# Optimization experiments

Hardware: AMD Instinct MI355X
Metric: run time of the kernel (lower is better)

Reference implementation:

```python
import jax, jax.numpy as jnp
import numpy as np

S, B, M, F, C = 32, 128, 128, 512, 100


def setup_inputs() -> dict:
    key = jax.random.key(0)
    k = jax.random.split(key, 7)
    x = jax.random.normal(k[0], (B, F), dtype=jnp.float32)
    y = jax.random.randint(k[1], (B,), 0, C, dtype=jnp.int32)
    # Z in {-1, +1}: Bernoulli(0.5) sample mapped via 2*b - 1 (mirrors sample_Z)
    Zb = (jax.random.uniform(k[2], (S, B, M)) < 0.5).astype(jnp.float32)
    Z = 2.0 * Zb - 1.0
    alpha_0 = jax.random.normal(k[3], (M,), dtype=jnp.float32)
    init_c = 2.0 / np.sqrt(F)
    alpha = init_c * jax.random.normal(k[4], (M, F), dtype=jnp.float32)
    alpha = alpha / jnp.linalg.norm(alpha, axis=0, keepdims=True)
    beta_0 = jax.random.normal(k[5], (C,), dtype=jnp.float32)
    init_c2 = 2.0 / np.sqrt(M)
    beta = init_c2 * jax.random.normal(k[6], (C, M), dtype=jnp.float32)
    return {"x": x, "y": y, "Z": Z, "alpha_0": alpha_0, "alpha": alpha,
            "beta_0": beta_0, "beta": beta}


def reference(x, y, Z, alpha_0, alpha, beta_0, beta):
    # linear_eta / eta (compute_linear_eta, compute_eta)
    linear_eta = alpha_0[None, :] + x @ alpha.T            # [B, M]
    eta = jax.nn.sigmoid(linear_eta)                        # exp(l)/(1+exp(l))

    y_onehot = jax.nn.one_hot(y, C, dtype=Z.dtype)          # [B, C]
    # Unperturbed logits shared across all j (rank-1 structure of compute_pi_j)
    base = beta_0[None, None, :] + jnp.einsum('sbm,cm->sbc', Z, beta)  # [S,B,C]

    def pi_for(target):
        # Flipping column j of Z to `target` shifts logits by (target - Z_j)*beta[:, j]
        delta = (target - Z)[..., None] * beta.T[None, None, :, :]  # [S,B,M,C]
        lin = base[:, :, None, :] + delta                            # [S,B,M,C]
        # NOTE: original ADDS the max (faithful to source); softmax ratio unchanged
        lin = lin + jnp.max(lin, axis=-1, keepdims=True)
        num = jnp.sum(y_onehot[None, :, None, :] * lin, axis=-1)     # [S,B,M]
        den = jnp.sum(jnp.exp(lin), axis=-1)                         # [S,B,M]
        return jnp.exp(num) / den                                    # [S,B,M]

    pi_pos = pi_for(1.0)
    pi_neg = pi_for(-1.0)
    # compute_EY_X_j: sum over Monte-Carlo samples
    EY_X_j = jnp.sum(pi_pos * eta[None] + pi_neg * (1.0 - eta)[None], axis=0)  # [B,M]
    return EY_X_j
```

## Files before the change

### kernel.cpp

```cpp
#include <hip/hip_runtime.h>
#include <math.h>

#define S_ 32
#define B_ 128
#define M_ 128
#define F_ 512
#define C_ 100
#define RWZ 136
#define RWE 120

typedef _Float16 f16;
typedef _Float16 f16x2 __attribute__((ext_vector_type(2)));
typedef _Float16 f16x4 __attribute__((ext_vector_type(4)));
typedef _Float16 f16x8 __attribute__((ext_vector_type(8)));
typedef float f32x4 __attribute__((ext_vector_type(4)));

__global__ __launch_bounds__(512) void k_main(
    const float* __restrict__ x, const int* __restrict__ y,
    const float* __restrict__ Z, const float* __restrict__ alpha0,
    const float* __restrict__ alpha, const float* __restrict__ beta0,
    const float* __restrict__ beta, float* __restrict__ out) {
  const int b = blockIdx.x;
  const int tid = threadIdx.x;
  const int lane = tid & 63;
  const int w = tid >> 6;
  const int l15 = lane & 15;
  const int lg = lane >> 4;

  __shared__ f16 Zf[S_ * RWZ];
  __shared__ f16 BT[112 * RWZ];
  __shared__ f16 EPT[M_ * RWE];
  __shared__ f16 ENT[M_ * RWE];
  __shared__ float baseS[S_ * 112];
  __shared__ f16 Pt[S_ * RWE];
  __shared__ float etaS[M_];
  __shared__ float PybS[S_];

  const int yb = y[b];

  {
    const float4* Z4 = (const float4*)Z;
#pragma unroll
    for (int i4 = tid; i4 < 1024; i4 += 512) {
      int p = i4 >> 5;
      int mj = (i4 & 31) * 4;
      float4 v = Z4[((size_t)p * B_ + b) * 32 + (i4 & 31)];
      f16x4 h = {(f16)v.x, (f16)v.y, (f16)v.z, (f16)v.w};
      *(f16x4*)&Zf[p * RWZ + mj] = h;
    }
    const float4* be4 = (const float4*)beta;
    for (int i4 = tid; i4 < 3200; i4 += 512) {
      int c = i4 >> 5;
      int mj = (i4 & 31) * 4;
      float4 v = be4[i4];
      f16x4 h = {(f16)v.x, (f16)v.y, (f16)v.z, (f16)v.w};
      *(f16x4*)&BT[c * RWZ + mj] = h;
    }
    for (int i = tid; i < 12 * RWZ; i += 512) BT[100 * RWZ + i] = (f16)0.f;
  }
  __syncthreads();

  {
    for (int i = tid; i < 8192; i += 512) {
      int c = i & 127;
      int m2 = (i >> 7) << 1;
      if (c < 112) {
        float ep0 = 0.f, en0 = 0.f, ep1 = 0.f, en1 = 0.f;
        if (c < C_) {
          f16x2 bb = *(const f16x2*)&BT[c * RWZ + m2];
          float b0 = (float)bb[0], b1 = (float)bb[1];
          ep0 = __expf(2.f * b0); en0 = __expf(-2.f * b0);
          ep1 = __expf(2.f * b1); en1 = __expf(-2.f * b1);
        }
        EPT[m2 * RWE + c] = (f16)ep0; EPT[(m2 + 1) * RWE + c] = (f16)ep1;
        ENT[m2 * RWE + c] = (f16)en0; ENT[(m2 + 1) * RWE + c] = (f16)en1;
      }
    }
    const float4* x4 = (const float4*)x;
    const float4* a4 = (const float4*)alpha;
    float4 xr[8];
#pragma unroll
    for (int r = 0; r < 8; ++r) xr[r] = x4[b * 128 + r * 16 + l15];
#pragma unroll
    for (int j = 0; j < 4; ++j) {
      int m = w * 16 + j * 4 + lg;
      float acc = 0.f;
#pragma unroll
      for (int r = 0; r < 8; ++r) {
        float4 av = a4[(size_t)m * 128 + r * 16 + l15];
        float4 xv = xr[r];
        acc = fmaf(av.x, xv.x, acc); acc = fmaf(av.y, xv.y, acc);
        acc = fmaf(av.z, xv.z, acc); acc = fmaf(av.w, xv.w, acc);
      }
      acc += __shfl_xor(acc, 1);
      acc += __shfl_xor(acc, 2);
      acc += __shfl_xor(acc, 4);
      acc += __shfl_xor(acc, 8);
      if (l15 == 0) {
        float l = alpha0[m] + acc;
        etaS[m] = 1.f / (1.f + __expf(-l));
      }
    }
  }
  __syncthreads();

  if (w < 7) {
    f32x4 acc0 = {0.f, 0.f, 0.f, 0.f}, acc1 = {0.f, 0.f, 0.f, 0.f};
    const char* ZfB = (const char*)Zf;
    const char* BTB = (const char*)BT;
#pragma unroll
    for (int kc = 0; kc < 4; ++kc) {
      int ko = kc * 64 + lg * 16;
      f16x8 a0 = *(const f16x8*)(ZfB + l15 * (RWZ * 2) + ko);
      f16x8 a1 = *(const f16x8*)(ZfB + (16 + l15) * (RWZ * 2) + ko);
      f16x8 bb = *(const f16x8*)(BTB + (w * 16 + l15) * (RWZ * 2) + ko);
      acc0 = __builtin_amdgcn_mfma_f32_16x16x32_f16(a0, bb, acc0, 0, 0, 0);
      acc1 = __builtin_amdgcn_mfma_f32_16x16x32_f16(a1, bb, acc1, 0, 0, 0);
    }
    int col = w * 16 + l15;
    float b0v = (col < C_) ? beta0[col] : 0.f;
#pragma unroll
    for (int j = 0; j < 4; ++j) {
      baseS[(lg * 4 + j) * 112 + col] = acc0[j] + b0v;
      baseS[(16 + lg * 4 + j) * 112 + col] = acc1[j] + b0v;
    }
  }
  __syncthreads();

  {
#pragma unroll
    for (int k = 0; k < 4; ++k) {
      int p = w * 4 + k;
      float v1 = baseS[p * 112 + lane];
      float v2 = (lane < 36) ? baseS[p * 112 + 64 + lane] : -1e30f;
      float mx = fmaxf(v1, v2);
#pragma unroll
      for (int off = 32; off > 0; off >>= 1) mx = fmaxf(mx, __shfl_xor(mx, off));
      float e1 = __expf(v1 - mx);
      float e2 = (lane < 36) ? __expf(v2 - mx) : 0.f;
      float sm = e1 + e2;
#pragma unroll
      for (int off = 32; off > 0; off >>= 1) sm += __shfl_xor(sm, off);
      float rd = 1.f / sm;
      Pt[p * RWE + lane] = (f16)(e1 * rd);
      if (lane < 48) Pt[p * RWE + 64 + lane] = (f16)(lane < 36 ? e2 * rd : 0.f);
      if (lane == yb) PybS[p] = e1 * rd;
      if (lane + 64 == yb) PybS[p] = e2 * rd;
    }
  }
  __syncthreads();

  {
    f32x4 pAcc0 = {0.f,0.f,0.f,0.f}, pAcc1 = {0.f,0.f,0.f,0.f};
    f32x4 nAcc0 = {0.f,0.f,0.f,0.f}, nAcc1 = {0.f,0.f,0.f,0.f};
    const char* PtB = (const char*)Pt;
    const char* EPB = (const char*)EPT;
    const char* ENB = (const char*)ENT;
#pragma unroll
    for (int kc = 0; kc < 3; ++kc) {
      int ko = kc * 64 + lg * 16;
      f16x8 a0 = *(const f16x8*)(PtB + l15 * (RWE * 2) + ko);
      f16x8 a1 = *(const f16x8*)(PtB + (16 + l15) * (RWE * 2) + ko);
      f16x8 bp = *(const f16x8*)(EPB + (w * 16 + l15) * (RWE * 2) + ko);
      f16x8 bn = *(const f16x8*)(ENB + (w * 16 + l15) * (RWE * 2) + ko);
      pAcc0 = __builtin_amdgcn_mfma_f32_16x16x32_f16(a0, bp, pAcc0, 0, 0, 0);
      pAcc1 = __builtin_amdgcn_mfma_f32_16x16x32_f16(a1, bp, pAcc1, 0, 0, 0);
      nAcc0 = __builtin_amdgcn_mfma_f32_16x16x32_f16(a0, bn, nAcc0, 0, 0, 0);
      nAcc1 = __builtin_amdgcn_mfma_f32_16x16x32_f16(a1, bn, nAcc1, 0, 0, 0);
    }
    {
      int ko3 = 192 + lg * 8;
      f16x4 a0 = *(const f16x4*)(PtB + l15 * (RWE * 2) + ko3);
      f16x4 a1 = *(const f16x4*)(PtB + (16 + l15) * (RWE * 2) + ko3);
      f16x4 bp = *(const f16x4*)(EPB + (w * 16 + l15) * (RWE * 2) + ko3);
      f16x4 bn = *(const f16x4*)(ENB + (w * 16 + l15) * (RWE * 2) + ko3);
      pAcc0 = __builtin_amdgcn_mfma_f32_16x16x16f16(a0, bp, pAcc0, 0, 0, 0);
      pAcc1 = __builtin_amdgcn_mfma_f32_16x16x16f16(a1, bp, pAcc1, 0, 0, 0);
      nAcc0 = __builtin_amdgcn_mfma_f32_16x16x16f16(a0, bn, nAcc0, 0, 0, 0);
      nAcc1 = __builtin_amdgcn_mfma_f32_16x16x16f16(a1, bn, nAcc1, 0, 0, 0);
    }
    int m = w * 16 + l15;
    float epy = (float)EPT[m * RWE + yb];
    float eny = (float)ENT[m * RWE + yb];
    float eta_v = etaS[m];
    float ome = 1.f - eta_v;
    float o = 0.f;
#pragma unroll
    for (int j = 0; j < 4; ++j) {
      {
        int p = lg * 4 + j;
        float z = (float)Zf[p * RWZ + m];
        float pyb = PybS[p];
        o += (z > 0.f) ? fmaf(pyb, eta_v, (pyb * eny / nAcc0[j]) * ome)
                       : fmaf(pyb * epy / pAcc0[j], eta_v, pyb * ome);
      }
      {
        int p = 16 + lg * 4 + j;
        float z = (float)Zf[p * RWZ + m];
        float pyb = PybS[p];
        o += (z > 0.f) ? fmaf(pyb, eta_v, (pyb * eny / nAcc1[j]) * ome)
                       : fmaf(pyb * epy / pAcc1[j], eta_v, pyb * ome);
      }
    }
    o += __shfl_xor(o, 16);
    o += __shfl_xor(o, 32);
    if (lane < 16) out[b * M_ + w * 16 + lane] = o;
  }
}

extern "C" void kernel_launch(void* const* d_in, const int* in_sizes, int n_in,
                              void* d_out, int out_size, void* d_ws, size_t ws_size,
                              hipStream_t stream) {
  const float* x = (const float*)d_in[0];
  const int* y = (const int*)d_in[1];
  const float* Z = (const float*)d_in[2];
  const float* alpha0 = (const float*)d_in[3];
  const float* alpha = (const float*)d_in[4];
  const float* beta0 = (const float*)d_in[5];
  const float* beta = (const float*)d_in[6];
  float* out = (float*)d_out;

  k_main<<<dim3(B_), dim3(512), 0, stream>>>(x, y, Z, alpha0, alpha, beta0,
                                             beta, out);
}
```

Baseline: 17.77 us.

## Split into precompute kernel and S-split main kernel with atomic accumulation

Moves the beta-to-f16 conversion, the exp(±2β) tables and the eta computation out of the per-batch block into a separate pre-kernel that writes them to workspace, so they are computed once instead of once per block. The main kernel is then split across two blocks per batch row, each handling 16 samples, and the two halves are combined with atomicAdd into an output zeroed by a memset. This doubles the grid and shrinks shared memory per block, which should help occupancy. The cost is two extra launches (memset and pre-kernel), a workspace round-trip, reading the B tables from global memory instead of LDS, and atomics on the output.

```diff
diff --git a/kernel.cpp b/kernel.cpp
--- a/kernel.cpp
+++ b/kernel.cpp
@@ -15,72 +15,25 @@
 typedef _Float16 f16x8 __attribute__((ext_vector_type(8)));
 typedef float f32x4 __attribute__((ext_vector_type(4)));
 
-__global__ __launch_bounds__(512) void k_main(
-    const float* __restrict__ x, const int* __restrict__ y,
-    const float* __restrict__ Z, const float* __restrict__ alpha0,
-    const float* __restrict__ alpha, const float* __restrict__ beta0,
-    const float* __restrict__ beta, float* __restrict__ out) {
-  const int b = blockIdx.x;
+#define WS_BT   0
+#define WS_EPT  30720
+#define WS_ENT  61440
+#define WS_ETA  92160
+
+__global__ __launch_bounds__(512) void k_pre(
+    const float* __restrict__ x, const float* __restrict__ alpha0,
+    const float* __restrict__ alpha, const float* __restrict__ beta,
+    char* __restrict__ ws) {
+  const int bid = blockIdx.x;
   const int tid = threadIdx.x;
-  const int lane = tid & 63;
-  const int w = tid >> 6;
-  const int l15 = lane & 15;
-  const int lg = lane >> 4;
-
-  __shared__ f16 Zf[S_ * RWZ];
-  __shared__ f16 BT[112 * RWZ];
-  __shared__ f16 EPT[M_ * RWE];
-  __shared__ f16 ENT[M_ * RWE];
-  __shared__ float baseS[S_ * 112];
-  __shared__ f16 Pt[S_ * RWE];
-  __shared__ float etaS[M_];
-  __shared__ float PybS[S_];
-
-  const int yb = y[b];
-
-  {
-    const float4* Z4 = (const float4*)Z;
-#pragma unroll
-    for (int i4 = tid; i4 < 1024; i4 += 512) {
-      int p = i4 >> 5;
-      int mj = (i4 & 31) * 4;
-      float4 v = Z4[((size_t)p * B_ + b) * 32 + (i4 & 31)];
-      f16x4 h = {(f16)v.x, (f16)v.y, (f16)v.z, (f16)v.w};
-      *(f16x4*)&Zf[p * RWZ + mj] = h;
-    }
-    const float4* be4 = (const float4*)beta;
-    for (int i4 = tid; i4 < 3200; i4 += 512) {
-      int c = i4 >> 5;
-      int mj = (i4 & 31) * 4;
-      float4 v = be4[i4];
-      f16x4 h = {(f16)v.x, (f16)v.y, (f16)v.z, (f16)v.w};
-      *(f16x4*)&BT[c * RWZ + mj] = h;
-    }
-    for (int i = tid; i < 12 * RWZ; i += 512) BT[100 * RWZ + i] = (f16)0.f;
-  }
-  __syncthreads();
-
-  {
-    for (int i = tid; i < 8192; i += 512) {
-      int c = i & 127;
-      int m2 = (i >> 7) << 1;
-      if (c < 112) {
-        float ep0 = 0.f, en0 = 0.f, ep1 = 0.f, en1 = 0.f;
-        if (c < C_) {
-          f16x2 bb = *(const f16x2*)&BT[c * RWZ + m2];
-          float b0 = (float)bb[0], b1 = (float)bb[1];
-          ep0 = __expf(2.f * b0); en0 = __expf(-2.f * b0);
-          ep1 = __expf(2.f * b1); en1 = __expf(-2.f * b1);
-        }
-        EPT[m2 * RWE + c] = (f16)ep0; EPT[(m2 + 1) * RWE + c] = (f16)ep1;
-        ENT[m2 * RWE + c] = (f16)en0; ENT[(m2 + 1) * RWE + c] = (f16)en1;
-      }
-    }
+  if (bid < B_) {
+    float* etag = (float*)(ws + WS_ETA);
+    const int lane = tid & 63, w = tid >> 6, l15 = lane & 15, lg = lane >> 4;
     const float4* x4 = (const float4*)x;
     const float4* a4 = (const float4*)alpha;
     float4 xr[8];
 #pragma unroll
-    for (int r = 0; r < 8; ++r) xr[r] = x4[b * 128 + r * 16 + l15];
+    for (int r = 0; r < 8; ++r) xr[r] = x4[bid * 128 + r * 16 + l15];
 #pragma unroll
     for (int j = 0; j < 4; ++j) {
       int m = w * 16 + j * 4 + lg;
@@ -98,39 +51,85 @@
       acc += __shfl_xor(acc, 8);
       if (l15 == 0) {
         float l = alpha0[m] + acc;
-        etaS[m] = 1.f / (1.f + __expf(-l));
+        etag[bid * 128 + m] = 1.f / (1.f + __expf(-l));
       }
     }
+  } else {
+    f16* BTg = (f16*)(ws + WS_BT);
+    f16* EPTg = (f16*)(ws + WS_EPT);
+    f16* ENTg = (f16*)(ws + WS_ENT);
+    const int base = (bid - B_) * 512;
+    for (int i = base + tid; i < C_ * M_; i += 4 * 512) {
+      int c = i >> 7, m = i & 127;
+      float bv = beta[i];
+      BTg[c * RWZ + m] = (f16)bv;
+      EPTg[m * RWE + c] = (f16)__expf(2.f * bv);
+      ENTg[m * RWE + c] = (f16)__expf(-2.f * bv);
+    }
+    for (int i = base + tid; i < 12 * RWZ; i += 4 * 512) BTg[100 * RWZ + i] = (f16)0.f;
+    for (int i = base + tid; i < 128 * 32; i += 4 * 512) {
+      int m = i >> 5, k = i & 31;
+      if (k < 20) { EPTg[m * RWE + 100 + k] = (f16)0.f; ENTg[m * RWE + 100 + k] = (f16)0.f; }
+    }
+  }
+}
+
+__global__ __launch_bounds__(512) void k_main(
+    const float* __restrict__ Z, const int* __restrict__ y,
+    const float* __restrict__ beta0, const char* __restrict__ ws,
+    float* __restrict__ out) {
+  const int sh = blockIdx.x;
+  const int b = blockIdx.y;
+  const int tid = threadIdx.x;
+  const int lane = tid & 63;
+  const int w = tid >> 6;
+  const int l15 = lane & 15;
+  const int lg = lane >> 4;
+
+  const f16* BTg = (const f16*)(ws + WS_BT);
+  const f16* EPTg = (const f16*)(ws + WS_EPT);
+  const f16* ENTg = (const f16*)(ws + WS_ENT);
+  const float* etag = (const float*)(ws + WS_ETA);
+
+  __shared__ f16 Zf[16 * RWZ];
+  __shared__ float baseS[16 * 112];
+  __shared__ f16 Pt[16 * RWE];
+  __shared__ float PybS[16];
+
+  const int yb = y[b];
+
+  {
+    int p = tid >> 5, q = tid & 31;
+    float4 v = ((const float4*)Z)[((size_t)(sh * 16 + p) * B_ + b) * 32 + q];
+    f16x4 h = {(f16)v.x, (f16)v.y, (f16)v.z, (f16)v.w};
+    *(f16x4*)&Zf[p * RWZ + q * 4] = h;
   }
   __syncthreads();
 
   if (w < 7) {
-    f32x4 acc0 = {0.f, 0.f, 0.f, 0.f}, acc1 = {0.f, 0.f, 0.f, 0.f};
+    const char* BTB = (const char*)BTg;
     const char* ZfB = (const char*)Zf;
-    const char* BTB = (const char*)BT;
+    f16x8 bfr[4];
+#pragma unroll
+    for (int kc = 0; kc < 4; ++kc)
+      bfr[kc] = *(const f16x8*)(BTB + (w * 16 + l15) * (RWZ * 2) + kc * 64 + lg * 16);
+    f32x4 acc = {0.f, 0.f, 0.f, 0.f};
 #pragma unroll
     for (int kc = 0; kc < 4; ++kc) {
-      int ko = kc * 64 + lg * 16;
-      f16x8 a0 = *(const f16x8*)(ZfB + l15 * (RWZ * 2) + ko);
-      f16x8 a1 = *(const f16x8*)(ZfB + (16 + l15) * (RWZ * 2) + ko);
-      f16x8 bb = *(const f16x8*)(BTB + (w * 16 + l15) * (RWZ * 2) + ko);
-      acc0 = __builtin_amdgcn_mfma_f32_16x16x32_f16(a0, bb, acc0, 0, 0, 0);
-      acc1 = __builtin_amdgcn_mfma_f32_16x16x32_f16(a1, bb, acc1, 0, 0, 0);
+      f16x8 a0 = *(const f16x8*)(ZfB + l15 * (RWZ * 2) + kc * 64 + lg * 16);
+      acc = __builtin_amdgcn_mfma_f32_16x16x32_f16(a0, bfr[kc], acc, 0, 0, 0);
     }
     int col = w * 16 + l15;
     float b0v = (col < C_) ? beta0[col] : 0.f;
 #pragma unroll
-    for (int j = 0; j < 4; ++j) {
-      baseS[(lg * 4 + j) * 112 + col] = acc0[j] + b0v;
-      baseS[(16 + lg * 4 + j) * 112 + col] = acc1[j] + b0v;
-    }
+    for (int j = 0; j < 4; ++j) baseS[(lg * 4 + j) * 112 + col] = acc[j] + b0v;
   }
   __syncthreads();
 
   {
 #pragma unroll
-    for (int k = 0; k < 4; ++k) {
-      int p = w * 4 + k;
+    for (int k = 0; k < 2; ++k) {
+      int p = w * 2 + k;
       float v1 = baseS[p * 112 + lane];
       float v2 = (lane < 36) ? baseS[p * 112 + 64 + lane] : -1e30f;
       float mx = fmaxf(v1, v2);
@@ -151,60 +150,47 @@
   __syncthreads();
 
   {
-    f32x4 pAcc0 = {0.f,0.f,0.f,0.f}, pAcc1 = {0.f,0.f,0.f,0.f};
-    f32x4 nAcc0 = {0.f,0.f,0.f,0.f}, nAcc1 = {0.f,0.f,0.f,0.f};
     const char* PtB = (const char*)Pt;
-    const char* EPB = (const char*)EPT;
-    const char* ENB = (const char*)ENT;
+    const char* EPB = (const char*)EPTg;
+    const char* ENB = (const char*)ENTg;
+    const int rowoff = (w * 16 + l15) * (RWE * 2);
+    f16x8 bp[3], bn[3];
 #pragma unroll
     for (int kc = 0; kc < 3; ++kc) {
-      int ko = kc * 64 + lg * 16;
-      f16x8 a0 = *(const f16x8*)(PtB + l15 * (RWE * 2) + ko);
-      f16x8 a1 = *(const f16x8*)(PtB + (16 + l15) * (RWE * 2) + ko);
-      f16x8 bp = *(const f16x8*)(EPB + (w * 16 + l15) * (RWE * 2) + ko);
-      f16x8 bn = *(const f16x8*)(ENB + (w * 16 + l15) * (RWE * 2) + ko);
-      pAcc0 = __builtin_amdgcn_mfma_f32_16x16x32_f16(a0, bp, pAcc0, 0, 0, 0);
-      pAcc1 = __builtin_amdgcn_mfma_f32_16x16x32_f16(a1, bp, pAcc1, 0, 0, 0);
-      nAcc0 = __builtin_amdgcn_mfma_f32_16x16x32_f16(a0, bn, nAcc0, 0, 0, 0);
-      nAcc1 = __builtin_amdgcn_mfma_f32_16x16x32_f16(a1, bn, nAcc1, 0, 0, 0);
+      bp[kc] = *(const f16x8*)(EPB + rowoff + kc * 64 + lg * 16);
+      bn[kc] = *(const f16x8*)(ENB + rowoff + kc * 64 + lg * 16);
+    }
+    f16x4 bp3 = *(const f16x4*)(EPB + rowoff + 192 + lg * 8);
+    f16x4 bn3 = *(const f16x4*)(ENB + rowoff + 192 + lg * 8);
+    f32x4 pA = {0.f, 0.f, 0.f, 0.f}, nA = {0.f, 0.f, 0.f, 0.f};
+#pragma unroll
+    for (int kc = 0; kc < 3; ++kc) {
+      f16x8 a0 = *(const f16x8*)(PtB + l15 * (RWE * 2) + kc * 64 + lg * 16);
+      pA = __builtin_amdgcn_mfma_f32_16x16x32_f16(a0, bp[kc], pA, 0, 0, 0);
+      nA = __builtin_amdgcn_mfma_f32_16x16x32_f16(a0, bn[kc], nA, 0, 0, 0);
     }
     {
-      int ko3 = 192 + lg * 8;
-      f16x4 a0 = *(const f16x4*)(PtB + l15 * (RWE * 2) + ko3);
-      f16x4 a1 = *(const f16x4*)(PtB + (16 + l15) * (RWE * 2) + ko3);
-      f16x4 bp = *(const f16x4*)(EPB + (w * 16 + l15) * (RWE * 2) + ko3);
-      f16x4 bn = *(const f16x4*)(ENB + (w * 16 + l15) * (RWE * 2) + ko3);
-      pAcc0 = __builtin_amdgcn_mfma_f32_16x16x16f16(a0, bp, pAcc0, 0, 0, 0);
-      pAcc1 = __builtin_amdgcn_mfma_f32_16x16x16f16(a1, bp, pAcc1, 0, 0, 0);
-      nAcc0 = __builtin_amdgcn_mfma_f32_16x16x16f16(a0, bn, nAcc0, 0, 0, 0);
-      nAcc1 = __builtin_amdgcn_mfma_f32_16x16x16f16(a1, bn, nAcc1, 0, 0, 0);
+      f16x4 a3 = *(const f16x4*)(PtB + l15 * (RWE * 2) + 192 + lg * 8);
+      pA = __builtin_amdgcn_mfma_f32_16x16x16f16(a3, bp3, pA, 0, 0, 0);
+      nA = __builtin_amdgcn_mfma_f32_16x16x16f16(a3, bn3, nA, 0, 0, 0);
     }
     int m = w * 16 + l15;
-    float epy = (float)EPT[m * RWE + yb];
-    float eny = (float)ENT[m * RWE + yb];
-    float eta_v = etaS[m];
+    float epy = (float)EPTg[m * RWE + yb];
+    float eny = (float)ENTg[m * RWE + yb];
+    float eta_v = etag[b * M_ + m];
     float ome = 1.f - eta_v;
     float o = 0.f;
 #pragma unroll
     for (int j = 0; j < 4; ++j) {
-      {
-        int p = lg * 4 + j;
-        float z = (float)Zf[p * RWZ + m];
-        float pyb = PybS[p];
-        o += (z > 0.f) ? fmaf(pyb, eta_v, (pyb * eny / nAcc0[j]) * ome)
-                       : fmaf(pyb * epy / pAcc0[j], eta_v, pyb * ome);
-      }
-      {
-        int p = 16 + lg * 4 + j;
-        float z = (float)Zf[p * RWZ + m];
-        float pyb = PybS[p];
-        o += (z > 0.f) ? fmaf(pyb, eta_v, (pyb * eny / nAcc1[j]) * ome)
-                       : fmaf(pyb * epy / pAcc1[j], eta_v, pyb * ome);
-      }
+      int p = lg * 4 + j;
+      float z = (float)Zf[p * RWZ + m];
+      float pyb = PybS[p];
+      o += (z > 0.f) ? fmaf(pyb, eta_v, (pyb * eny / nA[j]) * ome)
+                     : fmaf(pyb * epy / pA[j], eta_v, pyb * ome);
     }
     o += __shfl_xor(o, 16);
     o += __shfl_xor(o, 32);
-    if (lane < 16) out[b * M_ + w * 16 + lane] = o;
+    if (lane < 16) atomicAdd(&out[b * M_ + w * 16 + lane], o);
   }
 }
 
@@ -219,7 +205,9 @@
   const float* beta0 = (const float*)d_in[5];
   const float* beta = (const float*)d_in[6];
   float* out = (float*)d_out;
-
-  k_main<<<dim3(B_), dim3(512), 0, stream>>>(x, y, Z, alpha0, alpha, beta0,
-                                             beta, out);
+  char* ws = (char*)d_ws;
+
+  hipMemsetAsync(out, 0, (size_t)B_ * M_ * sizeof(float), stream);
+  k_pre<<<dim3(B_ + 4), dim3(512), 0, stream>>>(x, alpha0, alpha, beta, ws);
+  k_main<<<dim3(2, B_), dim3(512), 0, stream>>>(Z, y, beta0, ws, out);
 }
```

Result: slower. 20.81 us (+17.1%).

## Precompute beta fragments and exp tables in pre-kernel, load MFMA operands from workspace

Applied to the files above, without the earlier changes.

Adds a small preprocessing kernel that converts beta to fp16 and computes exp(±2·beta), writing them to the workspace already laid out in MFMA fragment order. The main kernel now loads these B operands straight into registers from global memory instead of having each of the 128 blocks rebuild the beta copy and the exp tables in shared memory. This removes redundant per-block exp work, a barrier and a large amount of LDS, which may allow more blocks per CU. The cost is an extra kernel launch plus global reads of the fragments from each block. The final M-contraction is padded to a uniform K of 128, which drops the special-case K=16 tail.

```diff
diff --git a/kernel.cpp b/kernel.cpp
--- a/kernel.cpp
+++ b/kernel.cpp
@@ -7,19 +7,67 @@
 #define F_ 512
 #define C_ 100
 #define RWZ 136
-#define RWE 120
+#define RWP 136
 
 typedef _Float16 f16;
-typedef _Float16 f16x2 __attribute__((ext_vector_type(2)));
 typedef _Float16 f16x4 __attribute__((ext_vector_type(4)));
 typedef _Float16 f16x8 __attribute__((ext_vector_type(8)));
 typedef float f32x4 __attribute__((ext_vector_type(4)));
+
+#define WS_BT 0
+#define WS_EP 28672
+#define WS_EN 61440
+
+__global__ __launch_bounds__(512) void k_pre(const float* __restrict__ beta,
+                                             char* __restrict__ ws) {
+  __shared__ float betaS[C_ * M_];
+  const int tid = threadIdx.x;
+  for (int i = tid; i < C_ * M_; i += 512) betaS[i] = beta[i];
+  __syncthreads();
+  const int ci = blockIdx.x * 512 + tid;
+  if (ci < 1792) {
+    int lane = ci & 63, t = ci >> 6;
+    int rt = t % 7, kc = t / 7;
+    int c = rt * 16 + (lane & 15);
+    int m0 = kc * 32 + (lane >> 4) * 8;
+    f16x8 v;
+#pragma unroll
+    for (int i = 0; i < 8; ++i)
+      v[i] = (c < C_) ? (f16)betaS[c * M_ + m0 + i] : (f16)0.f;
+    *(f16x8*)(ws + WS_BT + (size_t)ci * 16) = v;
+  } else if (ci < 3840) {
+    int q = ci - 1792;
+    int lane = q & 63, t = q >> 6;
+    int m = (t & 7) * 16 + (lane & 15);
+    int c0 = (t >> 3) * 32 + (lane >> 4) * 8;
+    f16x8 v;
+#pragma unroll
+    for (int i = 0; i < 8; ++i) {
+      int c = c0 + i;
+      v[i] = (c < C_) ? (f16)__expf(2.f * betaS[c * M_ + m]) : (f16)0.f;
+    }
+    *(f16x8*)(ws + WS_EP + (size_t)q * 16) = v;
+  } else if (ci < 5888) {
+    int q = ci - 3840;
+    int lane = q & 63, t = q >> 6;
+    int m = (t & 7) * 16 + (lane & 15);
+    int c0 = (t >> 3) * 32 + (lane >> 4) * 8;
+    f16x8 v;
+#pragma unroll
+    for (int i = 0; i < 8; ++i) {
+      int c = c0 + i;
+      v[i] = (c < C_) ? (f16)__expf(-2.f * betaS[c * M_ + m]) : (f16)0.f;
+    }
+    *(f16x8*)(ws + WS_EN + (size_t)q * 16) = v;
+  }
+}
 
 __global__ __launch_bounds__(512) void k_main(
     const float* __restrict__ x, const int* __restrict__ y,
     const float* __restrict__ Z, const float* __restrict__ alpha0,
     const float* __restrict__ alpha, const float* __restrict__ beta0,
-    const float* __restrict__ beta, float* __restrict__ out) {
+    const float* __restrict__ beta, const char* __restrict__ ws,
+    float* __restrict__ out) {
   const int b = blockIdx.x;
   const int tid = threadIdx.x;
   const int lane = tid & 63;
@@ -28,53 +76,22 @@
   const int lg = lane >> 4;
 
   __shared__ f16 Zf[S_ * RWZ];
-  __shared__ f16 BT[112 * RWZ];
-  __shared__ f16 EPT[M_ * RWE];
-  __shared__ f16 ENT[M_ * RWE];
   __shared__ float baseS[S_ * 112];
-  __shared__ f16 Pt[S_ * RWE];
+  __shared__ f16 Pt[S_ * RWP];
+  __shared__ float PybS[S_];
   __shared__ float etaS[M_];
-  __shared__ float PybS[S_];
 
   const int yb = y[b];
 
   {
     const float4* Z4 = (const float4*)Z;
 #pragma unroll
-    for (int i4 = tid; i4 < 1024; i4 += 512) {
-      int p = i4 >> 5;
-      int mj = (i4 & 31) * 4;
-      float4 v = Z4[((size_t)p * B_ + b) * 32 + (i4 & 31)];
+    for (int k = 0; k < 2; ++k) {
+      int i4 = tid + k * 512;
+      int p = i4 >> 5, q = i4 & 31;
+      float4 v = Z4[((size_t)p * B_ + b) * 32 + q];
       f16x4 h = {(f16)v.x, (f16)v.y, (f16)v.z, (f16)v.w};
-      *(f16x4*)&Zf[p * RWZ + mj] = h;
-    }
-    const float4* be4 = (const float4*)beta;
-    for (int i4 = tid; i4 < 3200; i4 += 512) {
-      int c = i4 >> 5;
-      int mj = (i4 & 31) * 4;
-      float4 v = be4[i4];
-      f16x4 h = {(f16)v.x, (f16)v.y, (f16)v.z, (f16)v.w};
-      *(f16x4*)&BT[c * RWZ + mj] = h;
-    }
-    for (int i = tid; i < 12 * RWZ; i += 512) BT[100 * RWZ + i] = (f16)0.f;
-  }
-  __syncthreads();
-
-  {
-    for (int i = tid; i < 8192; i += 512) {
-      int c = i & 127;
-      int m2 = (i >> 7) << 1;
-      if (c < 112) {
-        float ep0 = 0.f, en0 = 0.f, ep1 = 0.f, en1 = 0.f;
-        if (c < C_) {
-          f16x2 bb = *(const f16x2*)&BT[c * RWZ + m2];
-          float b0 = (float)bb[0], b1 = (float)bb[1];
-          ep0 = __expf(2.f * b0); en0 = __expf(-2.f * b0);
-          ep1 = __expf(2.f * b1); en1 = __expf(-2.f * b1);
-        }
-        EPT[m2 * RWE + c] = (f16)ep0; EPT[(m2 + 1) * RWE + c] = (f16)ep1;
-        ENT[m2 * RWE + c] = (f16)en0; ENT[(m2 + 1) * RWE + c] = (f16)en1;
-      }
+      *(f16x4*)&Zf[p * RWZ + q * 4] = h;
     }
     const float4* x4 = (const float4*)x;
     const float4* a4 = (const float4*)alpha;
@@ -105,17 +122,18 @@
   __syncthreads();
 
   if (w < 7) {
+    f16x8 bfr[4];
+#pragma unroll
+    for (int kc = 0; kc < 4; ++kc)
+      bfr[kc] = *(const f16x8*)(ws + WS_BT + (size_t)((kc * 7 + w) * 64 + lane) * 16);
     f32x4 acc0 = {0.f, 0.f, 0.f, 0.f}, acc1 = {0.f, 0.f, 0.f, 0.f};
     const char* ZfB = (const char*)Zf;
-    const char* BTB = (const char*)BT;
 #pragma unroll
     for (int kc = 0; kc < 4; ++kc) {
-      int ko = kc * 64 + lg * 16;
-      f16x8 a0 = *(const f16x8*)(ZfB + l15 * (RWZ * 2) + ko);
-      f16x8 a1 = *(const f16x8*)(ZfB + (16 + l15) * (RWZ * 2) + ko);
-      f16x8 bb = *(const f16x8*)(BTB + (w * 16 + l15) * (RWZ * 2) + ko);
-      acc0 = __builtin_amdgcn_mfma_f32_16x16x32_f16(a0, bb, acc0, 0, 0, 0);
-      acc1 = __builtin_amdgcn_mfma_f32_16x16x32_f16(a1, bb, acc1, 0, 0, 0);
+      f16x8 a0 = *(const f16x8*)(ZfB + l15 * (RWZ * 2) + kc * 64 + lg * 16);
+      f16x8 a1 = *(const f16x8*)(ZfB + (16 + l15) * (RWZ * 2) + kc * 64 + lg * 16);
+      acc0 = __builtin_amdgcn_mfma_f32_16x16x32_f16(a0, bfr[kc], acc0, 0, 0, 0);
+      acc1 = __builtin_amdgcn_mfma_f32_16x16x32_f16(a1, bfr[kc], acc1, 0, 0, 0);
     }
     int col = w * 16 + l15;
     float b0v = (col < C_) ? beta0[col] : 0.f;
@@ -142,8 +160,8 @@
 #pragma unroll
       for (int off = 32; off > 0; off >>= 1) sm += __shfl_xor(sm, off);
       float rd = 1.f / sm;
-      Pt[p * RWE + lane] = (f16)(e1 * rd);
-      if (lane < 48) Pt[p * RWE + 64 + lane] = (f16)(lane < 36 ? e2 * rd : 0.f);
+      Pt[p * RWP + lane] = (f16)(e1 * rd);
+      Pt[p * RWP + 64 + lane] = (f16)((lane < 36) ? e2 * rd : 0.f);
       if (lane == yb) PybS[p] = e1 * rd;
       if (lane + 64 == yb) PybS[p] = e2 * rd;
     }
@@ -151,37 +169,27 @@
   __syncthreads();
 
   {
-    f32x4 pAcc0 = {0.f,0.f,0.f,0.f}, pAcc1 = {0.f,0.f,0.f,0.f};
-    f32x4 nAcc0 = {0.f,0.f,0.f,0.f}, nAcc1 = {0.f,0.f,0.f,0.f};
+    f16x8 bp[4], bn[4];
+#pragma unroll
+    for (int kc = 0; kc < 4; ++kc) {
+      bp[kc] = *(const f16x8*)(ws + WS_EP + (size_t)((kc * 8 + w) * 64 + lane) * 16);
+      bn[kc] = *(const f16x8*)(ws + WS_EN + (size_t)((kc * 8 + w) * 64 + lane) * 16);
+    }
+    f32x4 pA0 = {0.f,0.f,0.f,0.f}, pA1 = {0.f,0.f,0.f,0.f};
+    f32x4 nA0 = {0.f,0.f,0.f,0.f}, nA1 = {0.f,0.f,0.f,0.f};
     const char* PtB = (const char*)Pt;
-    const char* EPB = (const char*)EPT;
-    const char* ENB = (const char*)ENT;
-#pragma unroll
-    for (int kc = 0; kc < 3; ++kc) {
-      int ko = kc * 64 + lg * 16;
-      f16x8 a0 = *(const f16x8*)(PtB + l15 * (RWE * 2) + ko);
-      f16x8 a1 = *(const f16x8*)(PtB + (16 + l15) * (RWE * 2) + ko);
-      f16x8 bp = *(const f16x8*)(EPB + (w * 16 + l15) * (RWE * 2) + ko);
-      f16x8 bn = *(const f16x8*)(ENB + (w * 16 + l15) * (RWE * 2) + ko);
-      pAcc0 = __builtin_amdgcn_mfma_f32_16x16x32_f16(a0, bp, pAcc0, 0, 0, 0);
-      pAcc1 = __builtin_amdgcn_mfma_f32_16x16x32_f16(a1, bp, pAcc1, 0, 0, 0);
-      nAcc0 = __builtin_amdgcn_mfma_f32_16x16x32_f16(a0, bn, nAcc0, 0, 0, 0);
-      nAcc1 = __builtin_amdgcn_mfma_f32_16x16x32_f16(a1, bn, nAcc1, 0, 0, 0);
-    }
-    {
-      int ko3 = 192 + lg * 8;
-      f16x4 a0 = *(const f16x4*)(PtB + l15 * (RWE * 2) + ko3);
-      f16x4 a1 = *(const f16x4*)(PtB + (16 + l15) * (RWE * 2) + ko3);
-      f16x4 bp = *(const f16x4*)(EPB + (w * 16 + l15) * (RWE * 2) + ko3);
-      f16x4 bn = *(const f16x4*)(ENB + (w * 16 + l15) * (RWE * 2) + ko3);
-      pAcc0 = __builtin_amdgcn_mfma_f32_16x16x16f16(a0, bp, pAcc0, 0, 0, 0);
-      pAcc1 = __builtin_amdgcn_mfma_f32_16x16x16f16(a1, bp, pAcc1, 0, 0, 0);
-      nAcc0 = __builtin_amdgcn_mfma_f32_16x16x16f16(a0, bn, nAcc0, 0, 0, 0);
-      nAcc1 = __builtin_amdgcn_mfma_f32_16x16x16f16(a1, bn, nAcc1, 0, 0, 0);
+#pragma unroll
+    for (int kc = 0; kc < 4; ++kc) {
+      f16x8 a0 = *(const f16x8*)(PtB + l15 * (RWP * 2) + kc * 64 + lg * 16);
+      f16x8 a1 = *(const f16x8*)(PtB + (16 + l15) * (RWP * 2) + kc * 64 + lg * 16);
+      pA0 = __builtin_amdgcn_mfma_f32_16x16x32_f16(a0, bp[kc], pA0, 0, 0, 0);
+      nA0 = __builtin_amdgcn_mfma_f32_16x16x32_f16(a0, bn[kc], nA0, 0, 0, 0);
+      pA1 = __builtin_amdgcn_mfma_f32_16x16x32_f16(a1, bp[kc], pA1, 0, 0, 0);
+      nA1 = __builtin_amdgcn_mfma_f32_16x16x32_f16(a1, bn[kc], nA1, 0, 0, 0);
     }
     int m = w * 16 + l15;
-    float epy = (float)EPT[m * RWE + yb];
-    float eny = (float)ENT[m * RWE + yb];
+    float bym = beta[yb * M_ + m];
+    float epy = __expf(2.f * bym), eny = __expf(-2.f * bym);
     float eta_v = etaS[m];
     float ome = 1.f - eta_v;
     float o = 0.f;
@@ -191,20 +199,20 @@
         int p = lg * 4 + j;
         float z = (float)Zf[p * RWZ + m];
         float pyb = PybS[p];
-        o += (z > 0.f) ? fmaf(pyb, eta_v, (pyb * eny / nAcc0[j]) * ome)
-                       : fmaf(pyb * epy / pAcc0[j], eta_v, pyb * ome);
+        o += (z > 0.f) ? fmaf(pyb, eta_v, (pyb * eny / nA0[j]) * ome)
+                       : fmaf(pyb * epy / pA0[j], eta_v, pyb * ome);
       }
       {
         int p = 16 + lg * 4 + j;
         float z = (float)Zf[p * RWZ + m];
         float pyb = PybS[p];
-        o += (z > 0.f) ? fmaf(pyb, eta_v, (pyb * eny / nAcc1[j]) * ome)
-                       : fmaf(pyb * epy / pAcc1[j], eta_v, pyb * ome);
+        o += (z > 0.f) ? fmaf(pyb, eta_v, (pyb * eny / nA1[j]) * ome)
+                       : fmaf(pyb * epy / pA1[j], eta_v, pyb * ome);
       }
     }
     o += __shfl_xor(o, 16);
     o += __shfl_xor(o, 32);
-    if (lane < 16) out[b * M_ + w * 16 + lane] = o;
+    if (lane < 16) out[b * M_ + w * 16 + l15] = o;
   }
 }
 
@@ -219,7 +227,9 @@
   const float* beta0 = (const float*)d_in[5];
   const float* beta = (const float*)d_in[6];
   float* out = (float*)d_out;
-
+  char* ws = (char*)d_ws;
+
+  k_pre<<<dim3(12), dim3(512), 0, stream>>>(beta, ws);
   k_main<<<dim3(B_), dim3(512), 0, stream>>>(x, y, Z, alpha0, alpha, beta0,
-                                             beta, out);
+                                             beta, ws, out);
 }
```

Result: slower. 19.25 us (+8.4%).
